# Performance work log

Measured on AMD Instinct MI355X. Metric: run time of the kernel, lower is better.

## Reference

```python
import jax, jax.numpy as jnp
import numpy as np

B, C, N = 4, 512, 4096
CQK = C // 8

def setup_inputs() -> dict:
    key = jax.random.key(0)
    ks = jax.random.split(key, 8)
    s = 0.02  # weight init scale
    return {
        "x": jax.random.normal(ks[0], (B, C, N), dtype=jnp.float32),
        "Wq": jax.random.normal(ks[1], (CQK, C), dtype=jnp.float32) * s,
        "bq": jax.random.normal(ks[2], (CQK,), dtype=jnp.float32) * s,
        "Wk": jax.random.normal(ks[3], (CQK, C), dtype=jnp.float32) * s,
        "bk": jax.random.normal(ks[4], (CQK,), dtype=jnp.float32) * s,
        "Wv": jax.random.normal(ks[5], (C, C), dtype=jnp.float32) * s,
        "bv": jax.random.normal(ks[6], (C,), dtype=jnp.float32) * s,
        "gamma": jax.random.normal(ks[7], (1,), dtype=jnp.float32),
    }

def reference(x, Wq, bq, Wk, bk, Wv, bv, gamma):
    # pointwise Conv1d == per-point matmul: [B,C,N] -> [B,Cout,N]
    q = jnp.einsum('oc,bcn->bon', Wq, x) + bq[None, :, None]   # [B,CQK,N]
    k = jnp.einsum('oc,bcn->bon', Wk, x) + bk[None, :, None]   # [B,CQK,N]
    v = jnp.einsum('oc,bcn->bon', Wv, x) + bv[None, :, None]   # [B,C,N]
    # attention[b,i,j] = sum_c q[b,c,i] * k[b,c,j]  (unscaled, non-causal)
    attn = jnp.einsum('bci,bcj->bij', q, k)                    # [B,N,N]
    attn = jax.nn.softmax(attn, axis=-1)
    # out[b,c,i] = sum_j v[b,c,j] * attn[b,i,j]
    out = jnp.einsum('bcj,bij->bci', v, attn)                  # [B,C,N]
    return gamma[0] * out + x
```

## Files before the change

kernel.cpp:

```cpp
#include <hip/hip_runtime.h>
#include <math.h>

#define B_ 4
#define C_ 512
#define N_ 4096
#define LOG2E 1.44269504088896f

typedef __attribute__((ext_vector_type(8))) short s8v;
typedef __attribute__((ext_vector_type(4))) float f4v;

#define MF32(a, b, c) __builtin_amdgcn_mfma_f32_16x16x32_bf16(a, b, c, 0, 0, 0)

#if defined(__has_builtin) && __has_builtin(__builtin_amdgcn_exp2f)
#define EXP2(x) __builtin_amdgcn_exp2f(x)
#else
#define EXP2(x) exp2f(x)
#endif

#define BARRIER_LDS() do {                                   \
    __builtin_amdgcn_sched_barrier(0);                       \
    asm volatile("s_waitcnt lgkmcnt(0)" ::: "memory");       \
    __builtin_amdgcn_s_barrier();                            \
    __builtin_amdgcn_sched_barrier(0);                       \
} while (0)

static __device__ __forceinline__ ushort f2bf(float f) {
    unsigned u = __float_as_uint(f);
    u += 0x7FFFu + ((u >> 16) & 1u);
    return (ushort)(u >> 16);
}

__global__ __launch_bounds__(256) void wconv_kernel(
    const float* __restrict__ Wq, const float* __restrict__ Wk,
    const float* __restrict__ Wv, ushort* __restrict__ Wb)
{
    const int row = blockIdx.x;
    const float* src = row < 64 ? Wq + (size_t)row * C_
                     : row < 128 ? Wk + (size_t)(row - 64) * C_
                     : Wv + (size_t)(row - 128) * C_;
    const int t2 = threadIdx.x * 2;
    float2 v = *(const float2*)&src[t2];
    ushort2 o; o.x = f2bf(v.x); o.y = f2bf(v.y);
    *(ushort2*)&Wb[(size_t)row * C_ + t2] = o;
}

__global__ __launch_bounds__(512, 2) void qkv_fused(
    const float* __restrict__ x, const ushort* __restrict__ Wb,
    const float* __restrict__ bq, const float* __restrict__ bk,
    const float* __restrict__ bv,
    ushort* __restrict__ qT, ushort* __restrict__ kT, ushort* __restrict__ vB)
{
    extern __shared__ ushort Xs[];

    const int tid = threadIdx.x, w = tid >> 6, lane = tid & 63;
    const int li = lane & 15, qd = lane >> 4;
    const int n0 = blockIdx.x * 64, b = blockIdx.y;

    #pragma unroll
    for (int r = 0; r < 16; ++r) {
        const int f = r * 512 + tid;
        const int c = f >> 4;
        const int nch = f & 15;
        float4 v = *(const float4*)&x[((size_t)b * C_ + c) * N_ + n0 + nch * 4];
        const int n = nch * 4;
        Xs[((n + 0) * 512 + c) ^ (((n + 0) & 7) << 3)] = f2bf(v.x);
        Xs[((n + 1) * 512 + c) ^ (((n + 1) & 7) << 3)] = f2bf(v.y);
        Xs[((n + 2) * 512 + c) ^ (((n + 2) & 7) << 3)] = f2bf(v.z);
        Xs[((n + 3) * 512 + c) ^ (((n + 3) & 7) << 3)] = f2bf(v.w);
    }
    __syncthreads();

    const int rb0 = w * 80;
    const ushort* wrow[5];
    #pragma unroll
    for (int ot = 0; ot < 5; ++ot)
        wrow[ot] = Wb + (size_t)(rb0 + ot * 16 + li) * C_ + qd * 8;

    f4v acc[5][4];
    #pragma unroll
    for (int ot = 0; ot < 5; ++ot)
        #pragma unroll
        for (int nt = 0; nt < 4; ++nt)
            acc[ot][nt] = (f4v){0.f, 0.f, 0.f, 0.f};

    s8v awc[5], awn[5];
    #pragma unroll
    for (int ot = 0; ot < 5; ++ot)
        awc[ot] = *(const s8v*)(wrow[ot]);

    #pragma unroll 1
    for (int kc = 0; kc < C_; kc += 32) {
        const int kn = (kc + 32 < C_) ? kc + 32 : 0;
        #pragma unroll
        for (int ot = 0; ot < 5; ++ot)
            awn[ot] = *(const s8v*)(wrow[ot] + kn);

        s8v bx[4];
        #pragma unroll
        for (int nt = 0; nt < 4; ++nt) {
            const int n = nt * 16 + li;
            bx[nt] = *(const s8v*)&Xs[((n * 512) + kc + qd * 8) ^ ((li & 7) << 3)];
        }

        #pragma unroll
        for (int ot = 0; ot < 5; ++ot) {
            if (rb0 + ot * 16 >= 128) {
                #pragma unroll
                for (int nt = 0; nt < 4; ++nt)
                    acc[ot][nt] = MF32(bx[nt], awc[ot], acc[ot][nt]);
            } else {
                #pragma unroll
                for (int nt = 0; nt < 4; ++nt)
                    acc[ot][nt] = MF32(awc[ot], bx[nt], acc[ot][nt]);
            }
        }
        #pragma unroll
        for (int ot = 0; ot < 5; ++ot) awc[ot] = awn[ot];
    }

    #pragma unroll
    for (int ot = 0; ot < 5; ++ot) {
        const int rb = rb0 + ot * 16;
        if (rb < 128) {
            ushort* dst = rb < 64 ? qT : kT;
            const float* bias = rb < 64 ? bq : bk;
            const int ob = (rb < 64 ? rb : rb - 64) + qd * 4;
            const float sc = rb < 64 ? LOG2E : 1.0f;
            #pragma unroll
            for (int nt = 0; nt < 4; ++nt) {
                const int n = n0 + nt * 16 + li;
                ushort4 o;
                o.x = f2bf((acc[ot][nt][0] + bias[ob + 0]) * sc);
                o.y = f2bf((acc[ot][nt][1] + bias[ob + 1]) * sc);
                o.z = f2bf((acc[ot][nt][2] + bias[ob + 2]) * sc);
                o.w = f2bf((acc[ot][nt][3] + bias[ob + 3]) * sc);
                *(ushort4*)&dst[((size_t)b * N_ + n) * 64 + ob] = o;
            }
        } else {
            const int c = rb - 128 + li;
            const float bb = bv[c];
            #pragma unroll
            for (int nt = 0; nt < 4; ++nt) {
                const int n = n0 + nt * 16 + qd * 4;
                ushort4 o;
                o.x = f2bf(acc[ot][nt][0] + bb);
                o.y = f2bf(acc[ot][nt][1] + bb);
                o.z = f2bf(acc[ot][nt][2] + bb);
                o.w = f2bf(acc[ot][nt][3] + bb);
                *(ushort4*)&vB[((size_t)b * C_ + c) * N_ + n] = o;
            }
        }
    }
}

__device__ __forceinline__ void pv_chunk(
    const ushort* __restrict__ Pr, int li, int qd, int cidx,
    const s8v* vf, f4v (&acc)[4][8])
{
    const int sw = li & 7;
    #pragma unroll
    for (int h = 0; h < 2; ++h) {
        s8v pf[4];
        #pragma unroll
        for (int g = 0; g < 4; ++g)
            pf[g] = *(const s8v*)&Pr[(size_t)((h * 4 + g) * 16 + li) * 256
                                     + (((cidx * 4 + qd) ^ sw) << 3)];
        #pragma unroll
        for (int ct = 0; ct < 4; ++ct)
            #pragma unroll
            for (int g = 0; g < 4; ++g)
                acc[ct][h * 4 + g] = MF32(vf[ct], pf[g], acc[ct][h * 4 + g]);
    }
}

__device__ __forceinline__ void s_phase(
    s8v ck0, s8v ck1, const s8v (&qf)[8][2], float (&lp)[8],
    ushort* __restrict__ Pw, int li, int qd, int chunkbase)
{
    const int off = (qd & 1) * 4;
    const int sw = li & 7;
    #pragma unroll
    for (int h = 0; h < 2; ++h) {
        f4v sac[4];
        #pragma unroll
        for (int g = 0; g < 4; ++g) {
            const int it = h * 4 + g;
            sac[g] = (f4v){0.f, 0.f, 0.f, 0.f};
            sac[g] = MF32(ck0, qf[it][0], sac[g]);
            sac[g] = MF32(ck1, qf[it][1], sac[g]);
        }
        #pragma unroll
        for (int g = 0; g < 4; ++g) {
            const int it = h * 4 + g;
            const float p0 = EXP2(sac[g][0]);
            const float p1 = EXP2(sac[g][1]);
            const float p2 = EXP2(sac[g][2]);
            const float p3 = EXP2(sac[g][3]);
            lp[it] += (p0 + p1) + (p2 + p3);
            unsigned r0, r1;
            asm("v_cvt_pk_bf16_f32 %0, %1, %2" : "=v"(r0) : "v"(p0), "v"(p1));
            asm("v_cvt_pk_bf16_f32 %0, %1, %2" : "=v"(r1) : "v"(p2), "v"(p3));
            uint2 u; u.x = r0; u.y = r1;
            *(uint2*)&Pw[(size_t)(it * 16 + li) * 256
                         + ((chunkbase ^ sw) << 3) + off] = u;
        }
    }
}

__global__ __launch_bounds__(512, 2) void attn_mfma(
    const ushort* __restrict__ qT, const ushort* __restrict__ kT,
    const ushort* __restrict__ vB, const float* __restrict__ x,
    const float* __restrict__ gamma, float* __restrict__ out)
{
    extern __shared__ char smem[];
    ushort* Pb0 = (ushort*)smem;
    ushort* Pb1 = (ushort*)(smem + 65536);
    float*  l_s = (float*)smem;

    const int tid = threadIdx.x, w = tid >> 6, lane = tid & 63;
    const int li = lane & 15, qd = lane >> 4;
    const int wg = blockIdx.x;
    const int i_base = (wg >> 3) * 128;
    const int combo = wg & 7;
    const int b = combo >> 1;
    const int c_base = (combo & 1) * 256;

    const ushort* qTb = qT + (size_t)b * N_ * 64;
    const ushort* kTb = kT + (size_t)b * N_ * 64;
    const ushort* vBb = vB + (size_t)b * C_ * N_;

    const int NT = N_ / 256;

    if (w < 4) {
        s8v qf[8][2];
        #pragma unroll
        for (int it = 0; it < 8; ++it)
            #pragma unroll
            for (int ks = 0; ks < 2; ++ks)
                qf[it][ks] = *(const s8v*)&qTb[(size_t)(i_base + it * 16 + li) * 64 + ks * 32 + qd * 8];
        float lp[8] = {0.f, 0.f, 0.f, 0.f, 0.f, 0.f, 0.f, 0.f};

        const ushort* kp[4];
        int cb[4];
        #pragma unroll
        for (int s = 0; s < 4; ++s) {
            kp[s] = kTb + (size_t)(w * 64 + s * 16 + li) * 64 + qd * 8;
            cb[s] = w * 8 + s * 2 + (qd >> 1);
        }

        s8v kn0[4], kn1[4];
        {
            s8v kc0[4], kc1[4];
            #pragma unroll
            for (int s = 0; s < 4; ++s) {
                kc0[s] = *(const s8v*)(kp[s]);
                kc1[s] = *(const s8v*)(kp[s] + 32);
            }
            #pragma unroll
            for (int s = 0; s < 4; ++s) {
                kn0[s] = *(const s8v*)(kp[s] + (size_t)256 * 64);
                kn1[s] = *(const s8v*)(kp[s] + (size_t)256 * 64 + 32);
            }
            #pragma unroll
            for (int s = 0; s < 4; ++s)
                s_phase(kc0[s], kc1[s], qf, lp, Pb0, li, qd, cb[s]);
        }
        BARRIER_LDS();

        #pragma unroll 1
        for (int t = 1; t < NT; ++t) {
            ushort* Pw = ((t - 1) & 1) ? Pb0 : Pb1;
            const size_t jnext = (t + 1 < NT) ? (size_t)(t + 1) * 256 : 0;
            #pragma unroll
            for (int s = 0; s < 4; ++s) {
                s8v c0 = kn0[s], c1 = kn1[s];
                kn0[s] = *(const s8v*)(kp[s] + jnext * 64);
                kn1[s] = *(const s8v*)(kp[s] + jnext * 64 + 32);
                s_phase(c0, c1, qf, lp, Pw, li, qd, cb[s]);
            }
            BARRIER_LDS();
        }

        #pragma unroll
        for (int it = 0; it < 8; ++it) {
            lp[it] += __shfl_xor(lp[it], 16, 64);
            lp[it] += __shfl_xor(lp[it], 32, 64);
        }
        if (qd == 0) {
            #pragma unroll
            for (int it = 0; it < 8; ++it) l_s[w * 128 + it * 16 + li] = lp[it];
        }
        BARRIER_LDS();
    } else {
        const int w2c = w - 4;
        f4v acc[4][8];
        #pragma unroll
        for (int ct = 0; ct < 4; ++ct)
            #pragma unroll
            for (int it = 0; it < 8; ++it)
                acc[ct][it] = (f4v){0.f, 0.f, 0.f, 0.f};

        const ushort* vptr[4];
        #pragma unroll
        for (int ct = 0; ct < 4; ++ct)
            vptr[ct] = vBb + (size_t)(c_base + w2c * 64 + ct * 16 + li) * N_ + qd * 8;

        s8v vr[2][4];
        #pragma unroll
        for (int sl = 0; sl < 2; ++sl)
            #pragma unroll
            for (int ct = 0; ct < 4; ++ct)
                vr[sl][ct] = *(const s8v*)(vptr[ct] + sl * 32);
        BARRIER_LDS();

        #pragma unroll 1
        for (int t = 1; t < NT; ++t) {
            const ushort* Pr = ((t - 1) & 1) ? Pb1 : Pb0;
            const size_t jprev = (size_t)(t - 1) * 256;
            const size_t jcur  = (size_t)t * 256;

            __builtin_amdgcn_s_setprio(1);
            #pragma unroll
            for (int c = 0; c < 8; ++c) {
                pv_chunk(Pr, li, qd, c, vr[c & 1], acc);
                const size_t jld = (c + 2 < 8) ? jprev + (size_t)(c + 2) * 32
                                               : jcur + (size_t)(c + 2 - 8) * 32;
                #pragma unroll
                for (int ct = 0; ct < 4; ++ct)
                    vr[c & 1][ct] = *(const s8v*)(vptr[ct] + jld);
            }
            __builtin_amdgcn_s_setprio(0);
            BARRIER_LDS();
        }

        {
            const ushort* Pr = ((NT - 2) & 1) ? Pb0 : Pb1;
            const size_t jprev = (size_t)(NT - 1) * 256;
            __builtin_amdgcn_s_setprio(1);
            #pragma unroll
            for (int c = 0; c < 8; ++c) {
                pv_chunk(Pr, li, qd, c, vr[c & 1], acc);
                if (c + 2 < 8) {
                    const size_t jld = jprev + (size_t)(c + 2) * 32;
                    #pragma unroll
                    for (int ct = 0; ct < 4; ++ct)
                        vr[c & 1][ct] = *(const s8v*)(vptr[ct] + jld);
                }
            }
            __builtin_amdgcn_s_setprio(0);
        }
        BARRIER_LDS();

        float inv[8];
        #pragma unroll
        for (int it = 0; it < 8; ++it) {
            float t = 0.f;
            #pragma unroll
            for (int ww = 0; ww < 4; ++ww) t += l_s[ww * 128 + it * 16 + li];
            inv[it] = 1.0f / t;
        }

        const float g = gamma[0];
        #pragma unroll
        for (int ct = 0; ct < 4; ++ct)
            #pragma unroll
            for (int it = 0; it < 8; ++it) {
                const int i = i_base + it * 16 + li;
                #pragma unroll
                for (int r = 0; r < 4; ++r) {
                    const int c = c_base + w2c * 64 + ct * 16 + qd * 4 + r;
                    const size_t off = ((size_t)b * C_ + c) * N_ + i;
                    out[off] = g * acc[ct][it][r] * inv[it] + x[off];
                }
            }
    }
}

extern "C" void kernel_launch(void* const* d_in, const int* in_sizes, int n_in,
                              void* d_out, int out_size, void* d_ws, size_t ws_size,
                              hipStream_t stream)
{
    const float* x     = (const float*)d_in[0];
    const float* Wq    = (const float*)d_in[1];
    const float* bq    = (const float*)d_in[2];
    const float* Wk    = (const float*)d_in[3];
    const float* bk    = (const float*)d_in[4];
    const float* Wv    = (const float*)d_in[5];
    const float* bv    = (const float*)d_in[6];
    const float* gamma = (const float*)d_in[7];
    float* out = (float*)d_out;

    ushort* vB = (ushort*)d_ws;
    ushort* qT = vB + (size_t)B_ * C_ * N_;
    ushort* kT = qT + (size_t)B_ * N_ * 64;
    ushort* Wb = kT + (size_t)B_ * N_ * 64;

    wconv_kernel<<<dim3(640), 256, 0, stream>>>(Wq, Wk, Wv, Wb);
    qkv_fused<<<dim3(N_ / 64, B_), 512, 65536, stream>>>(x, Wb, bq, bk, bv, qT, kT, vB);
    attn_mfma<<<dim3((N_ / 128) * 2 * B_), 512, 131072, stream>>>(qT, kT, vB, x, gamma, out);
}
```

Baseline: 208.5 us.

## Fuse weight conversion, QKV projection and attention into one cooperative kernel

Replaces the three separate launches (weight bf16 conversion, QKV projection, attention) with a single cooperative kernel of 256 workgroups that uses grid-wide syncs between phases. The goal is to remove two launch gaps and kernel tail effects. In exchange it adds two grid barriers, and every phase is forced into the same 256-block, 128 KB-LDS configuration, which means a single wave of blocks. The QKV phase now asks for 128 KB of LDS, which may lower occupancy compared with its original 64 KB launch.

```diff
diff --git a/kernel.cpp b/kernel.cpp
--- a/kernel.cpp
+++ b/kernel.cpp
@@ -1,5 +1,8 @@
 #include <hip/hip_runtime.h>
+#include <hip/hip_cooperative_groups.h>
 #include <math.h>
+
+namespace cg = cooperative_groups;
 
 #define B_ 4
 #define C_ 512
@@ -28,129 +31,6 @@
     unsigned u = __float_as_uint(f);
     u += 0x7FFFu + ((u >> 16) & 1u);
     return (ushort)(u >> 16);
-}
-
-__global__ __launch_bounds__(256) void wconv_kernel(
-    const float* __restrict__ Wq, const float* __restrict__ Wk,
-    const float* __restrict__ Wv, ushort* __restrict__ Wb)
-{
-    const int row = blockIdx.x;
-    const float* src = row < 64 ? Wq + (size_t)row * C_
-                     : row < 128 ? Wk + (size_t)(row - 64) * C_
-                     : Wv + (size_t)(row - 128) * C_;
-    const int t2 = threadIdx.x * 2;
-    float2 v = *(const float2*)&src[t2];
-    ushort2 o; o.x = f2bf(v.x); o.y = f2bf(v.y);
-    *(ushort2*)&Wb[(size_t)row * C_ + t2] = o;
-}
-
-__global__ __launch_bounds__(512, 2) void qkv_fused(
-    const float* __restrict__ x, const ushort* __restrict__ Wb,
-    const float* __restrict__ bq, const float* __restrict__ bk,
-    const float* __restrict__ bv,
-    ushort* __restrict__ qT, ushort* __restrict__ kT, ushort* __restrict__ vB)
-{
-    extern __shared__ ushort Xs[];
-
-    const int tid = threadIdx.x, w = tid >> 6, lane = tid & 63;
-    const int li = lane & 15, qd = lane >> 4;
-    const int n0 = blockIdx.x * 64, b = blockIdx.y;
-
-    #pragma unroll
-    for (int r = 0; r < 16; ++r) {
-        const int f = r * 512 + tid;
-        const int c = f >> 4;
-        const int nch = f & 15;
-        float4 v = *(const float4*)&x[((size_t)b * C_ + c) * N_ + n0 + nch * 4];
-        const int n = nch * 4;
-        Xs[((n + 0) * 512 + c) ^ (((n + 0) & 7) << 3)] = f2bf(v.x);
-        Xs[((n + 1) * 512 + c) ^ (((n + 1) & 7) << 3)] = f2bf(v.y);
-        Xs[((n + 2) * 512 + c) ^ (((n + 2) & 7) << 3)] = f2bf(v.z);
-        Xs[((n + 3) * 512 + c) ^ (((n + 3) & 7) << 3)] = f2bf(v.w);
-    }
-    __syncthreads();
-
-    const int rb0 = w * 80;
-    const ushort* wrow[5];
-    #pragma unroll
-    for (int ot = 0; ot < 5; ++ot)
-        wrow[ot] = Wb + (size_t)(rb0 + ot * 16 + li) * C_ + qd * 8;
-
-    f4v acc[5][4];
-    #pragma unroll
-    for (int ot = 0; ot < 5; ++ot)
-        #pragma unroll
-        for (int nt = 0; nt < 4; ++nt)
-            acc[ot][nt] = (f4v){0.f, 0.f, 0.f, 0.f};
-
-    s8v awc[5], awn[5];
-    #pragma unroll
-    for (int ot = 0; ot < 5; ++ot)
-        awc[ot] = *(const s8v*)(wrow[ot]);
-
-    #pragma unroll 1
-    for (int kc = 0; kc < C_; kc += 32) {
-        const int kn = (kc + 32 < C_) ? kc + 32 : 0;
-        #pragma unroll
-        for (int ot = 0; ot < 5; ++ot)
-            awn[ot] = *(const s8v*)(wrow[ot] + kn);
-
-        s8v bx[4];
-        #pragma unroll
-        for (int nt = 0; nt < 4; ++nt) {
-            const int n = nt * 16 + li;
-            bx[nt] = *(const s8v*)&Xs[((n * 512) + kc + qd * 8) ^ ((li & 7) << 3)];
-        }
-
-        #pragma unroll
-        for (int ot = 0; ot < 5; ++ot) {
-            if (rb0 + ot * 16 >= 128) {
-                #pragma unroll
-                for (int nt = 0; nt < 4; ++nt)
-                    acc[ot][nt] = MF32(bx[nt], awc[ot], acc[ot][nt]);
-            } else {
-                #pragma unroll
-                for (int nt = 0; nt < 4; ++nt)
-                    acc[ot][nt] = MF32(awc[ot], bx[nt], acc[ot][nt]);
-            }
-        }
-        #pragma unroll
-        for (int ot = 0; ot < 5; ++ot) awc[ot] = awn[ot];
-    }
-
-    #pragma unroll
-    for (int ot = 0; ot < 5; ++ot) {
-        const int rb = rb0 + ot * 16;
-        if (rb < 128) {
-            ushort* dst = rb < 64 ? qT : kT;
-            const float* bias = rb < 64 ? bq : bk;
-            const int ob = (rb < 64 ? rb : rb - 64) + qd * 4;
-            const float sc = rb < 64 ? LOG2E : 1.0f;
-            #pragma unroll
-            for (int nt = 0; nt < 4; ++nt) {
-                const int n = n0 + nt * 16 + li;
-                ushort4 o;
-                o.x = f2bf((acc[ot][nt][0] + bias[ob + 0]) * sc);
-                o.y = f2bf((acc[ot][nt][1] + bias[ob + 1]) * sc);
-                o.z = f2bf((acc[ot][nt][2] + bias[ob + 2]) * sc);
-                o.w = f2bf((acc[ot][nt][3] + bias[ob + 3]) * sc);
-                *(ushort4*)&dst[((size_t)b * N_ + n) * 64 + ob] = o;
-            }
-        } else {
-            const int c = rb - 128 + li;
-            const float bb = bv[c];
-            #pragma unroll
-            for (int nt = 0; nt < 4; ++nt) {
-                const int n = n0 + nt * 16 + qd * 4;
-                ushort4 o;
-                o.x = f2bf(acc[ot][nt][0] + bb);
-                o.y = f2bf(acc[ot][nt][1] + bb);
-                o.z = f2bf(acc[ot][nt][2] + bb);
-                o.w = f2bf(acc[ot][nt][3] + bb);
-                *(ushort4*)&vB[((size_t)b * C_ + c) * N_ + n] = o;
-            }
-        }
-    }
 }
 
 __device__ __forceinline__ void pv_chunk(
@@ -207,172 +87,305 @@
     }
 }
 
-__global__ __launch_bounds__(512, 2) void attn_mfma(
-    const ushort* __restrict__ qT, const ushort* __restrict__ kT,
-    const ushort* __restrict__ vB, const float* __restrict__ x,
-    const float* __restrict__ gamma, float* __restrict__ out)
+__global__ __launch_bounds__(512, 2) void fused_all(
+    const float* __restrict__ x,
+    const float* __restrict__ Wq, const float* __restrict__ bq,
+    const float* __restrict__ Wk, const float* __restrict__ bk,
+    const float* __restrict__ Wv, const float* __restrict__ bv,
+    const float* __restrict__ gamma, float* __restrict__ out,
+    ushort* __restrict__ qT, ushort* __restrict__ kT,
+    ushort* __restrict__ vB, ushort* __restrict__ Wb)
 {
     extern __shared__ char smem[];
-    ushort* Pb0 = (ushort*)smem;
-    ushort* Pb1 = (ushort*)(smem + 65536);
-    float*  l_s = (float*)smem;
-
-    const int tid = threadIdx.x, w = tid >> 6, lane = tid & 63;
+    cg::grid_group grid = cg::this_grid();
+
+    const int tid = threadIdx.x, wgid = blockIdx.x;
+    const int w = tid >> 6, lane = tid & 63;
     const int li = lane & 15, qd = lane >> 4;
-    const int wg = blockIdx.x;
-    const int i_base = (wg >> 3) * 128;
-    const int combo = wg & 7;
-    const int b = combo >> 1;
-    const int c_base = (combo & 1) * 256;
-
-    const ushort* qTb = qT + (size_t)b * N_ * 64;
-    const ushort* kTb = kT + (size_t)b * N_ * 64;
-    const ushort* vBb = vB + (size_t)b * C_ * N_;
-
-    const int NT = N_ / 256;
-
-    if (w < 4) {
-        s8v qf[8][2];
-        #pragma unroll
-        for (int it = 0; it < 8; ++it)
-            #pragma unroll
-            for (int ks = 0; ks < 2; ++ks)
-                qf[it][ks] = *(const s8v*)&qTb[(size_t)(i_base + it * 16 + li) * 64 + ks * 32 + qd * 8];
-        float lp[8] = {0.f, 0.f, 0.f, 0.f, 0.f, 0.f, 0.f, 0.f};
-
-        const ushort* kp[4];
-        int cb[4];
-        #pragma unroll
-        for (int s = 0; s < 4; ++s) {
-            kp[s] = kTb + (size_t)(w * 64 + s * 16 + li) * 64 + qd * 8;
-            cb[s] = w * 8 + s * 2 + (qd >> 1);
-        }
-
-        s8v kn0[4], kn1[4];
-        {
-            s8v kc0[4], kc1[4];
+
+    {
+        const int idx = wgid * 512 + tid;
+        #pragma unroll
+        for (int rep = 0; rep < 2; ++rep) {
+            const int i = idx + rep * (256 * 512);
+            if (i < 640 * 256) {
+                const int row = i >> 8;
+                const int cp = (i & 255) * 2;
+                const float* src = row < 64 ? Wq + (size_t)row * C_
+                                 : row < 128 ? Wk + (size_t)(row - 64) * C_
+                                 : Wv + (size_t)(row - 128) * C_;
+                float2 v = *(const float2*)&src[cp];
+                ushort2 o; o.x = f2bf(v.x); o.y = f2bf(v.y);
+                *(ushort2*)&Wb[(size_t)row * C_ + cp] = o;
+            }
+        }
+    }
+    __threadfence();
+    grid.sync();
+
+    {
+        ushort* Xs = (ushort*)smem;
+        const int n0 = (wgid & 63) * 64;
+        const int b = wgid >> 6;
+
+        #pragma unroll
+        for (int r = 0; r < 16; ++r) {
+            const int f = r * 512 + tid;
+            const int c = f >> 4;
+            const int nch = f & 15;
+            float4 v = *(const float4*)&x[((size_t)b * C_ + c) * N_ + n0 + nch * 4];
+            const int n = nch * 4;
+            Xs[((n + 0) * 512 + c) ^ (((n + 0) & 7) << 3)] = f2bf(v.x);
+            Xs[((n + 1) * 512 + c) ^ (((n + 1) & 7) << 3)] = f2bf(v.y);
+            Xs[((n + 2) * 512 + c) ^ (((n + 2) & 7) << 3)] = f2bf(v.z);
+            Xs[((n + 3) * 512 + c) ^ (((n + 3) & 7) << 3)] = f2bf(v.w);
+        }
+        __syncthreads();
+
+        const int rb0 = w * 80;
+        const ushort* wrow[5];
+        #pragma unroll
+        for (int ot = 0; ot < 5; ++ot)
+            wrow[ot] = Wb + (size_t)(rb0 + ot * 16 + li) * C_ + qd * 8;
+
+        f4v acc[5][4];
+        #pragma unroll
+        for (int ot = 0; ot < 5; ++ot)
+            #pragma unroll
+            for (int nt = 0; nt < 4; ++nt)
+                acc[ot][nt] = (f4v){0.f, 0.f, 0.f, 0.f};
+
+        s8v awc[5], awn[5];
+        #pragma unroll
+        for (int ot = 0; ot < 5; ++ot)
+            awc[ot] = *(const s8v*)(wrow[ot]);
+
+        #pragma unroll 1
+        for (int kc = 0; kc < C_; kc += 32) {
+            const int kn = (kc + 32 < C_) ? kc + 32 : 0;
+            #pragma unroll
+            for (int ot = 0; ot < 5; ++ot)
+                awn[ot] = *(const s8v*)(wrow[ot] + kn);
+
+            s8v bx[4];
+            #pragma unroll
+            for (int nt = 0; nt < 4; ++nt) {
+                const int n = nt * 16 + li;
+                bx[nt] = *(const s8v*)&Xs[((n * 512) + kc + qd * 8) ^ ((li & 7) << 3)];
+            }
+
+            #pragma unroll
+            for (int ot = 0; ot < 5; ++ot) {
+                if (rb0 + ot * 16 >= 128) {
+                    #pragma unroll
+                    for (int nt = 0; nt < 4; ++nt)
+                        acc[ot][nt] = MF32(bx[nt], awc[ot], acc[ot][nt]);
+                } else {
+                    #pragma unroll
+                    for (int nt = 0; nt < 4; ++nt)
+                        acc[ot][nt] = MF32(awc[ot], bx[nt], acc[ot][nt]);
+                }
+            }
+            #pragma unroll
+            for (int ot = 0; ot < 5; ++ot) awc[ot] = awn[ot];
+        }
+
+        #pragma unroll
+        for (int ot = 0; ot < 5; ++ot) {
+            const int rb = rb0 + ot * 16;
+            if (rb < 128) {
+                ushort* dst = rb < 64 ? qT : kT;
+                const float* bias = rb < 64 ? bq : bk;
+                const int ob = (rb < 64 ? rb : rb - 64) + qd * 4;
+                const float sc = rb < 64 ? LOG2E : 1.0f;
+                #pragma unroll
+                for (int nt = 0; nt < 4; ++nt) {
+                    const int n = n0 + nt * 16 + li;
+                    ushort4 o;
+                    o.x = f2bf((acc[ot][nt][0] + bias[ob + 0]) * sc);
+                    o.y = f2bf((acc[ot][nt][1] + bias[ob + 1]) * sc);
+                    o.z = f2bf((acc[ot][nt][2] + bias[ob + 2]) * sc);
+                    o.w = f2bf((acc[ot][nt][3] + bias[ob + 3]) * sc);
+                    *(ushort4*)&dst[((size_t)b * N_ + n) * 64 + ob] = o;
+                }
+            } else {
+                const int c = rb - 128 + li;
+                const float bb = bv[c];
+                #pragma unroll
+                for (int nt = 0; nt < 4; ++nt) {
+                    const int n = n0 + nt * 16 + qd * 4;
+                    ushort4 o;
+                    o.x = f2bf(acc[ot][nt][0] + bb);
+                    o.y = f2bf(acc[ot][nt][1] + bb);
+                    o.z = f2bf(acc[ot][nt][2] + bb);
+                    o.w = f2bf(acc[ot][nt][3] + bb);
+                    *(ushort4*)&vB[((size_t)b * C_ + c) * N_ + n] = o;
+                }
+            }
+        }
+    }
+    __threadfence();
+    grid.sync();
+
+    {
+        ushort* Pb0 = (ushort*)smem;
+        ushort* Pb1 = (ushort*)(smem + 65536);
+        float*  l_s = (float*)smem;
+
+        const int i_base = (wgid >> 3) * 128;
+        const int combo = wgid & 7;
+        const int b = combo >> 1;
+        const int c_base = (combo & 1) * 256;
+
+        const ushort* qTb = qT + (size_t)b * N_ * 64;
+        const ushort* kTb = kT + (size_t)b * N_ * 64;
+        const ushort* vBb = vB + (size_t)b * C_ * N_;
+
+        const int NT = N_ / 256;
+
+        if (w < 4) {
+            s8v qf[8][2];
+            #pragma unroll
+            for (int it = 0; it < 8; ++it)
+                #pragma unroll
+                for (int ks = 0; ks < 2; ++ks)
+                    qf[it][ks] = *(const s8v*)&qTb[(size_t)(i_base + it * 16 + li) * 64 + ks * 32 + qd * 8];
+            float lp[8] = {0.f, 0.f, 0.f, 0.f, 0.f, 0.f, 0.f, 0.f};
+
+            const ushort* kp[4];
+            int cb[4];
             #pragma unroll
             for (int s = 0; s < 4; ++s) {
-                kc0[s] = *(const s8v*)(kp[s]);
-                kc1[s] = *(const s8v*)(kp[s] + 32);
-            }
-            #pragma unroll
-            for (int s = 0; s < 4; ++s) {
-                kn0[s] = *(const s8v*)(kp[s] + (size_t)256 * 64);
-                kn1[s] = *(const s8v*)(kp[s] + (size_t)256 * 64 + 32);
-            }
-            #pragma unroll
-            for (int s = 0; s < 4; ++s)
-                s_phase(kc0[s], kc1[s], qf, lp, Pb0, li, qd, cb[s]);
-        }
-        BARRIER_LDS();
-
-        #pragma unroll 1
-        for (int t = 1; t < NT; ++t) {
-            ushort* Pw = ((t - 1) & 1) ? Pb0 : Pb1;
-            const size_t jnext = (t + 1 < NT) ? (size_t)(t + 1) * 256 : 0;
-            #pragma unroll
-            for (int s = 0; s < 4; ++s) {
-                s8v c0 = kn0[s], c1 = kn1[s];
-                kn0[s] = *(const s8v*)(kp[s] + jnext * 64);
-                kn1[s] = *(const s8v*)(kp[s] + jnext * 64 + 32);
-                s_phase(c0, c1, qf, lp, Pw, li, qd, cb[s]);
+                kp[s] = kTb + (size_t)(w * 64 + s * 16 + li) * 64 + qd * 8;
+                cb[s] = w * 8 + s * 2 + (qd >> 1);
+            }
+
+            s8v kn0[4], kn1[4];
+            {
+                s8v kc0[4], kc1[4];
+                #pragma unroll
+                for (int s = 0; s < 4; ++s) {
+                    kc0[s] = *(const s8v*)(kp[s]);
+                    kc1[s] = *(const s8v*)(kp[s] + 32);
+                }
+                #pragma unroll
+                for (int s = 0; s < 4; ++s) {
+                    kn0[s] = *(const s8v*)(kp[s] + (size_t)256 * 64);
+                    kn1[s] = *(const s8v*)(kp[s] + (size_t)256 * 64 + 32);
+                }
+                #pragma unroll
+                for (int s = 0; s < 4; ++s)
+                    s_phase(kc0[s], kc1[s], qf, lp, Pb0, li, qd, cb[s]);
             }
             BARRIER_LDS();
-        }
-
-        #pragma unroll
-        for (int it = 0; it < 8; ++it) {
-            lp[it] += __shfl_xor(lp[it], 16, 64);
-            lp[it] += __shfl_xor(lp[it], 32, 64);
-        }
-        if (qd == 0) {
-            #pragma unroll
-            for (int it = 0; it < 8; ++it) l_s[w * 128 + it * 16 + li] = lp[it];
-        }
-        BARRIER_LDS();
-    } else {
-        const int w2c = w - 4;
-        f4v acc[4][8];
-        #pragma unroll
-        for (int ct = 0; ct < 4; ++ct)
-            #pragma unroll
-            for (int it = 0; it < 8; ++it)
-                acc[ct][it] = (f4v){0.f, 0.f, 0.f, 0.f};
-
-        const ushort* vptr[4];
-        #pragma unroll
-        for (int ct = 0; ct < 4; ++ct)
-            vptr[ct] = vBb + (size_t)(c_base + w2c * 64 + ct * 16 + li) * N_ + qd * 8;
-
-        s8v vr[2][4];
-        #pragma unroll
-        for (int sl = 0; sl < 2; ++sl)
+
+            #pragma unroll 1
+            for (int t = 1; t < NT; ++t) {
+                ushort* Pw = ((t - 1) & 1) ? Pb0 : Pb1;
+                const size_t jnext = (t + 1 < NT) ? (size_t)(t + 1) * 256 : 0;
+                #pragma unroll
+                for (int s = 0; s < 4; ++s) {
+                    s8v c0 = kn0[s], c1 = kn1[s];
+                    kn0[s] = *(const s8v*)(kp[s] + jnext * 64);
+                    kn1[s] = *(const s8v*)(kp[s] + jnext * 64 + 32);
+                    s_phase(c0, c1, qf, lp, Pw, li, qd, cb[s]);
+                }
+                BARRIER_LDS();
+            }
+
+            #pragma unroll
+            for (int it = 0; it < 8; ++it) {
+                lp[it] += __shfl_xor(lp[it], 16, 64);
+                lp[it] += __shfl_xor(lp[it], 32, 64);
+            }
+            if (qd == 0) {
+                #pragma unroll
+                for (int it = 0; it < 8; ++it) l_s[w * 128 + it * 16 + li] = lp[it];
+            }
+            BARRIER_LDS();
+        } else {
+            const int w2c = w - 4;
+            f4v acc[4][8];
             #pragma unroll
             for (int ct = 0; ct < 4; ++ct)
-                vr[sl][ct] = *(const s8v*)(vptr[ct] + sl * 32);
-        BARRIER_LDS();
-
-        #pragma unroll 1
-        for (int t = 1; t < NT; ++t) {
-            const ushort* Pr = ((t - 1) & 1) ? Pb1 : Pb0;
-            const size_t jprev = (size_t)(t - 1) * 256;
-            const size_t jcur  = (size_t)t * 256;
-
-            __builtin_amdgcn_s_setprio(1);
-            #pragma unroll
-            for (int c = 0; c < 8; ++c) {
-                pv_chunk(Pr, li, qd, c, vr[c & 1], acc);
-                const size_t jld = (c + 2 < 8) ? jprev + (size_t)(c + 2) * 32
-                                               : jcur + (size_t)(c + 2 - 8) * 32;
+                #pragma unroll
+                for (int it = 0; it < 8; ++it)
+                    acc[ct][it] = (f4v){0.f, 0.f, 0.f, 0.f};
+
+            const ushort* vptr[4];
+            #pragma unroll
+            for (int ct = 0; ct < 4; ++ct)
+                vptr[ct] = vBb + (size_t)(c_base + w2c * 64 + ct * 16 + li) * N_ + qd * 8;
+
+            s8v vr[2][4];
+            #pragma unroll
+            for (int sl = 0; sl < 2; ++sl)
                 #pragma unroll
                 for (int ct = 0; ct < 4; ++ct)
-                    vr[c & 1][ct] = *(const s8v*)(vptr[ct] + jld);
-            }
-            __builtin_amdgcn_s_setprio(0);
+                    vr[sl][ct] = *(const s8v*)(vptr[ct] + sl * 32);
             BARRIER_LDS();
-        }
-
-        {
-            const ushort* Pr = ((NT - 2) & 1) ? Pb0 : Pb1;
-            const size_t jprev = (size_t)(NT - 1) * 256;
-            __builtin_amdgcn_s_setprio(1);
-            #pragma unroll
-            for (int c = 0; c < 8; ++c) {
-                pv_chunk(Pr, li, qd, c, vr[c & 1], acc);
-                if (c + 2 < 8) {
-                    const size_t jld = jprev + (size_t)(c + 2) * 32;
+
+            #pragma unroll 1
+            for (int t = 1; t < NT; ++t) {
+                const ushort* Pr = ((t - 1) & 1) ? Pb1 : Pb0;
+                const size_t jprev = (size_t)(t - 1) * 256;
+                const size_t jcur  = (size_t)t * 256;
+
+                __builtin_amdgcn_s_setprio(1);
+                #pragma unroll
+                for (int c = 0; c < 8; ++c) {
+                    pv_chunk(Pr, li, qd, c, vr[c & 1], acc);
+                    const size_t jld = (c + 2 < 8) ? jprev + (size_t)(c + 2) * 32
+                                                   : jcur + (size_t)(c + 2 - 8) * 32;
                     #pragma unroll
                     for (int ct = 0; ct < 4; ++ct)
                         vr[c & 1][ct] = *(const s8v*)(vptr[ct] + jld);
                 }
-            }
-            __builtin_amdgcn_s_setprio(0);
-        }
-        BARRIER_LDS();
-
-        float inv[8];
-        #pragma unroll
-        for (int it = 0; it < 8; ++it) {
-            float t = 0.f;
-            #pragma unroll
-            for (int ww = 0; ww < 4; ++ww) t += l_s[ww * 128 + it * 16 + li];
-            inv[it] = 1.0f / t;
-        }
-
-        const float g = gamma[0];
-        #pragma unroll
-        for (int ct = 0; ct < 4; ++ct)
+                __builtin_amdgcn_s_setprio(0);
+                BARRIER_LDS();
+            }
+
+            {
+                const ushort* Pr = ((NT - 2) & 1) ? Pb0 : Pb1;
+                const size_t jprev = (size_t)(NT - 1) * 256;
+                __builtin_amdgcn_s_setprio(1);
+                #pragma unroll
+                for (int c = 0; c < 8; ++c) {
+                    pv_chunk(Pr, li, qd, c, vr[c & 1], acc);
+                    if (c + 2 < 8) {
+                        const size_t jld = jprev + (size_t)(c + 2) * 32;
+                        #pragma unroll
+                        for (int ct = 0; ct < 4; ++ct)
+                            vr[c & 1][ct] = *(const s8v*)(vptr[ct] + jld);
+                    }
+                }
+                __builtin_amdgcn_s_setprio(0);
+            }
+            BARRIER_LDS();
+
+            float inv[8];
             #pragma unroll
             for (int it = 0; it < 8; ++it) {
-                const int i = i_base + it * 16 + li;
-                #pragma unroll
-                for (int r = 0; r < 4; ++r) {
-                    const int c = c_base + w2c * 64 + ct * 16 + qd * 4 + r;
-                    const size_t off = ((size_t)b * C_ + c) * N_ + i;
-                    out[off] = g * acc[ct][it][r] * inv[it] + x[off];
-                }
-            }
+                float t = 0.f;
+                #pragma unroll
+                for (int ww = 0; ww < 4; ++ww) t += l_s[ww * 128 + it * 16 + li];
+                inv[it] = 1.0f / t;
+            }
+
+            const float g = gamma[0];
+            #pragma unroll
+            for (int ct = 0; ct < 4; ++ct)
+                #pragma unroll
+                for (int it = 0; it < 8; ++it) {
+                    const int i = i_base + it * 16 + li;
+                    #pragma unroll
+                    for (int r = 0; r < 4; ++r) {
+                        const int c = c_base + w2c * 64 + ct * 16 + qd * 4 + r;
+                        const size_t off = ((size_t)b * C_ + c) * N_ + i;
+                        out[off] = g * acc[ct][it][r] * inv[it] + x[off];
+                    }
+                }
+        }
     }
 }
 
@@ -395,7 +408,11 @@
     ushort* kT = qT + (size_t)B_ * N_ * 64;
     ushort* Wb = kT + (size_t)B_ * N_ * 64;
 
-    wconv_kernel<<<dim3(640), 256, 0, stream>>>(Wq, Wk, Wv, Wb);
-    qkv_fused<<<dim3(N_ / 64, B_), 512, 65536, stream>>>(x, Wb, bq, bk, bv, qT, kT, vB);
-    attn_mfma<<<dim3((N_ / 128) * 2 * B_), 512, 131072, stream>>>(qT, kT, vB, x, gamma, out);
+    void* kargs[] = {
+        (void*)&x, (void*)&Wq, (void*)&bq, (void*)&Wk, (void*)&bk,
+        (void*)&Wv, (void*)&bv, (void*)&gamma, (void*)&out,
+        (void*)&qT, (void*)&kT, (void*)&vB, (void*)&Wb };
+
+    hipLaunchCooperativeKernel((void*)fused_all, dim3(256), dim3(512),
+                               kargs, 131072, stream);
 }
```

New measurement: 380.6 us. +82.5%, slower.

## Halve attention query tile to 64 rows and raise occupancy to four blocks

Applied to the files above, without the earlier changes.

Shrinks the per-block query tile from 128 to 64 rows, which halves the LDS probability buffers (64KB total) and the accumulator registers, and doubles the grid. The launch bound now asks for 4 blocks per CU instead of 2. The V prefetch is reorganised into a two-register ping-pong inside each pair of chunks. The goal is higher occupancy and better latency hiding. The cost is that each block recomputes QK^T and exp for only half as many rows while still streaming all of K and V, so global traffic for K and V doubles, and the S-phase work per block drops relative to its fixed overheads.

```diff
diff --git a/kernel.cpp b/kernel.cpp
--- a/kernel.cpp
+++ b/kernel.cpp
@@ -155,72 +155,64 @@
 
 __device__ __forceinline__ void pv_chunk(
     const ushort* __restrict__ Pr, int li, int qd, int cidx,
-    const s8v* vf, f4v (&acc)[4][8])
+    const s8v* vf, f4v (&acc)[4][4])
 {
     const int sw = li & 7;
-    #pragma unroll
-    for (int h = 0; h < 2; ++h) {
-        s8v pf[4];
+    s8v pf[4];
+    #pragma unroll
+    for (int g = 0; g < 4; ++g)
+        pf[g] = *(const s8v*)&Pr[(size_t)(g * 16 + li) * 256
+                                 + (((cidx * 4 + qd) ^ sw) << 3)];
+    #pragma unroll
+    for (int ct = 0; ct < 4; ++ct)
         #pragma unroll
         for (int g = 0; g < 4; ++g)
-            pf[g] = *(const s8v*)&Pr[(size_t)((h * 4 + g) * 16 + li) * 256
-                                     + (((cidx * 4 + qd) ^ sw) << 3)];
-        #pragma unroll
-        for (int ct = 0; ct < 4; ++ct)
-            #pragma unroll
-            for (int g = 0; g < 4; ++g)
-                acc[ct][h * 4 + g] = MF32(vf[ct], pf[g], acc[ct][h * 4 + g]);
-    }
+            acc[ct][g] = MF32(vf[ct], pf[g], acc[ct][g]);
 }
 
 __device__ __forceinline__ void s_phase(
-    s8v ck0, s8v ck1, const s8v (&qf)[8][2], float (&lp)[8],
+    s8v ck0, s8v ck1, const s8v (&qf)[4][2], float (&lp)[4],
     ushort* __restrict__ Pw, int li, int qd, int chunkbase)
 {
     const int off = (qd & 1) * 4;
     const int sw = li & 7;
-    #pragma unroll
-    for (int h = 0; h < 2; ++h) {
-        f4v sac[4];
-        #pragma unroll
-        for (int g = 0; g < 4; ++g) {
-            const int it = h * 4 + g;
-            sac[g] = (f4v){0.f, 0.f, 0.f, 0.f};
-            sac[g] = MF32(ck0, qf[it][0], sac[g]);
-            sac[g] = MF32(ck1, qf[it][1], sac[g]);
-        }
-        #pragma unroll
-        for (int g = 0; g < 4; ++g) {
-            const int it = h * 4 + g;
-            const float p0 = EXP2(sac[g][0]);
-            const float p1 = EXP2(sac[g][1]);
-            const float p2 = EXP2(sac[g][2]);
-            const float p3 = EXP2(sac[g][3]);
-            lp[it] += (p0 + p1) + (p2 + p3);
-            unsigned r0, r1;
-            asm("v_cvt_pk_bf16_f32 %0, %1, %2" : "=v"(r0) : "v"(p0), "v"(p1));
-            asm("v_cvt_pk_bf16_f32 %0, %1, %2" : "=v"(r1) : "v"(p2), "v"(p3));
-            uint2 u; u.x = r0; u.y = r1;
-            *(uint2*)&Pw[(size_t)(it * 16 + li) * 256
-                         + ((chunkbase ^ sw) << 3) + off] = u;
-        }
-    }
-}
-
-__global__ __launch_bounds__(512, 2) void attn_mfma(
+    f4v sac[4];
+    #pragma unroll
+    for (int g = 0; g < 4; ++g) {
+        sac[g] = (f4v){0.f, 0.f, 0.f, 0.f};
+        sac[g] = MF32(ck0, qf[g][0], sac[g]);
+        sac[g] = MF32(ck1, qf[g][1], sac[g]);
+    }
+    #pragma unroll
+    for (int g = 0; g < 4; ++g) {
+        const float p0 = EXP2(sac[g][0]);
+        const float p1 = EXP2(sac[g][1]);
+        const float p2 = EXP2(sac[g][2]);
+        const float p3 = EXP2(sac[g][3]);
+        lp[g] += (p0 + p1) + (p2 + p3);
+        unsigned r0, r1;
+        asm("v_cvt_pk_bf16_f32 %0, %1, %2" : "=v"(r0) : "v"(p0), "v"(p1));
+        asm("v_cvt_pk_bf16_f32 %0, %1, %2" : "=v"(r1) : "v"(p2), "v"(p3));
+        uint2 u; u.x = r0; u.y = r1;
+        *(uint2*)&Pw[(size_t)(g * 16 + li) * 256
+                     + ((chunkbase ^ sw) << 3) + off] = u;
+    }
+}
+
+__global__ __launch_bounds__(512, 4) void attn_mfma(
     const ushort* __restrict__ qT, const ushort* __restrict__ kT,
     const ushort* __restrict__ vB, const float* __restrict__ x,
     const float* __restrict__ gamma, float* __restrict__ out)
 {
     extern __shared__ char smem[];
     ushort* Pb0 = (ushort*)smem;
-    ushort* Pb1 = (ushort*)(smem + 65536);
+    ushort* Pb1 = (ushort*)(smem + 32768);
     float*  l_s = (float*)smem;
 
     const int tid = threadIdx.x, w = tid >> 6, lane = tid & 63;
     const int li = lane & 15, qd = lane >> 4;
     const int wg = blockIdx.x;
-    const int i_base = (wg >> 3) * 128;
+    const int i_base = (wg >> 3) * 64;
     const int combo = wg & 7;
     const int b = combo >> 1;
     const int c_base = (combo & 1) * 256;
@@ -232,13 +224,13 @@
     const int NT = N_ / 256;
 
     if (w < 4) {
-        s8v qf[8][2];
-        #pragma unroll
-        for (int it = 0; it < 8; ++it)
+        s8v qf[4][2];
+        #pragma unroll
+        for (int it = 0; it < 4; ++it)
             #pragma unroll
             for (int ks = 0; ks < 2; ++ks)
                 qf[it][ks] = *(const s8v*)&qTb[(size_t)(i_base + it * 16 + li) * 64 + ks * 32 + qd * 8];
-        float lp[8] = {0.f, 0.f, 0.f, 0.f, 0.f, 0.f, 0.f, 0.f};
+        float lp[4] = {0.f, 0.f, 0.f, 0.f};
 
         const ushort* kp[4];
         int cb[4];
@@ -282,35 +274,33 @@
         }
 
         #pragma unroll
-        for (int it = 0; it < 8; ++it) {
+        for (int it = 0; it < 4; ++it) {
             lp[it] += __shfl_xor(lp[it], 16, 64);
             lp[it] += __shfl_xor(lp[it], 32, 64);
         }
         if (qd == 0) {
             #pragma unroll
-            for (int it = 0; it < 8; ++it) l_s[w * 128 + it * 16 + li] = lp[it];
+            for (int it = 0; it < 4; ++it) l_s[w * 64 + it * 16 + li] = lp[it];
         }
         BARRIER_LDS();
     } else {
         const int w2c = w - 4;
-        f4v acc[4][8];
+        f4v acc[4][4];
         #pragma unroll
         for (int ct = 0; ct < 4; ++ct)
             #pragma unroll
-            for (int it = 0; it < 8; ++it)
-                acc[ct][it] = (f4v){0.f, 0.f, 0.f, 0.f};
+            for (int g = 0; g < 4; ++g)
+                acc[ct][g] = (f4v){0.f, 0.f, 0.f, 0.f};
 
         const ushort* vptr[4];
         #pragma unroll
         for (int ct = 0; ct < 4; ++ct)
             vptr[ct] = vBb + (size_t)(c_base + w2c * 64 + ct * 16 + li) * N_ + qd * 8;
 
-        s8v vr[2][4];
-        #pragma unroll
-        for (int sl = 0; sl < 2; ++sl)
-            #pragma unroll
-            for (int ct = 0; ct < 4; ++ct)
-                vr[sl][ct] = *(const s8v*)(vptr[ct] + sl * 32);
+        s8v vA[4], vB_[4];
+        #pragma unroll
+        for (int ct = 0; ct < 4; ++ct)
+            vA[ct] = *(const s8v*)(vptr[ct]);
         BARRIER_LDS();
 
         #pragma unroll 1
@@ -321,13 +311,17 @@
 
             __builtin_amdgcn_s_setprio(1);
             #pragma unroll
-            for (int c = 0; c < 8; ++c) {
-                pv_chunk(Pr, li, qd, c, vr[c & 1], acc);
-                const size_t jld = (c + 2 < 8) ? jprev + (size_t)(c + 2) * 32
-                                               : jcur + (size_t)(c + 2 - 8) * 32;
+            for (int cp = 0; cp < 4; ++cp) {
                 #pragma unroll
                 for (int ct = 0; ct < 4; ++ct)
-                    vr[c & 1][ct] = *(const s8v*)(vptr[ct] + jld);
+                    vB_[ct] = *(const s8v*)(vptr[ct] + jprev + (size_t)(cp * 2 + 1) * 32);
+                pv_chunk(Pr, li, qd, cp * 2, vA, acc);
+                const size_t jld = (cp * 2 + 2 < 8)
+                                 ? jprev + (size_t)(cp * 2 + 2) * 32 : jcur;
+                #pragma unroll
+                for (int ct = 0; ct < 4; ++ct)
+                    vA[ct] = *(const s8v*)(vptr[ct] + jld);
+                pv_chunk(Pr, li, qd, cp * 2 + 1, vB_, acc);
             }
             __builtin_amdgcn_s_setprio(0);
             BARRIER_LDS();
@@ -338,39 +332,42 @@
             const size_t jprev = (size_t)(NT - 1) * 256;
             __builtin_amdgcn_s_setprio(1);
             #pragma unroll
-            for (int c = 0; c < 8; ++c) {
-                pv_chunk(Pr, li, qd, c, vr[c & 1], acc);
-                if (c + 2 < 8) {
-                    const size_t jld = jprev + (size_t)(c + 2) * 32;
+            for (int cp = 0; cp < 4; ++cp) {
+                #pragma unroll
+                for (int ct = 0; ct < 4; ++ct)
+                    vB_[ct] = *(const s8v*)(vptr[ct] + jprev + (size_t)(cp * 2 + 1) * 32);
+                pv_chunk(Pr, li, qd, cp * 2, vA, acc);
+                if (cp * 2 + 2 < 8) {
                     #pragma unroll
                     for (int ct = 0; ct < 4; ++ct)
-                        vr[c & 1][ct] = *(const s8v*)(vptr[ct] + jld);
+                        vA[ct] = *(const s8v*)(vptr[ct] + jprev + (size_t)(cp * 2 + 2) * 32);
                 }
+                pv_chunk(Pr, li, qd, cp * 2 + 1, vB_, acc);
             }
             __builtin_amdgcn_s_setprio(0);
         }
         BARRIER_LDS();
 
-        float inv[8];
-        #pragma unroll
-        for (int it = 0; it < 8; ++it) {
+        float inv[4];
+        #pragma unroll
+        for (int g = 0; g < 4; ++g) {
             float t = 0.f;
             #pragma unroll
-            for (int ww = 0; ww < 4; ++ww) t += l_s[ww * 128 + it * 16 + li];
-            inv[it] = 1.0f / t;
-        }
-
-        const float g = gamma[0];
+            for (int ww = 0; ww < 4; ++ww) t += l_s[ww * 64 + g * 16 + li];
+            inv[g] = 1.0f / t;
+        }
+
+        const float gmm = gamma[0];
         #pragma unroll
         for (int ct = 0; ct < 4; ++ct)
             #pragma unroll
-            for (int it = 0; it < 8; ++it) {
-                const int i = i_base + it * 16 + li;
+            for (int g = 0; g < 4; ++g) {
+                const int i = i_base + g * 16 + li;
                 #pragma unroll
                 for (int r = 0; r < 4; ++r) {
                     const int c = c_base + w2c * 64 + ct * 16 + qd * 4 + r;
                     const size_t off = ((size_t)b * C_ + c) * N_ + i;
-                    out[off] = g * acc[ct][it][r] * inv[it] + x[off];
+                    out[off] = gmm * acc[ct][g][r] * inv[g] + x[off];
                 }
             }
     }
@@ -397,5 +394,5 @@
 
     wconv_kernel<<<dim3(640), 256, 0, stream>>>(Wq, Wk, Wv, Wb);
     qkv_fused<<<dim3(N_ / 64, B_), 512, 65536, stream>>>(x, Wb, bq, bk, bv, qT, kT, vB);
-    attn_mfma<<<dim3((N_ / 128) * 2 * B_), 512, 131072, stream>>>(qT, kT, vB, x, gamma, out);
-}
+    attn_mfma<<<dim3((N_ / 64) * 2 * B_), 512, 65536, stream>>>(qT, kT, vB, x, gamma, out);
+}
```

Result: slower. 295.1 us (+41.5%).
